# Optimization experiments

Measured on AMD Instinct MI355X. Metric: run time of the kernel, lower is better.

Reference implementation:

```python
import jax, jax.numpy as jnp
import numpy as np

DIM = 4096
NH = 32       # query heads
NKV = 8       # kv heads
HD = DIM // NH  # 128
B = 1
S = 2048
ROPE_BASE = 10000.0


def rope_tables(seq_len, head_dim, base=ROPE_BASE):
    inv_freq = 1.0 / base ** (jnp.arange(0, head_dim, 2, dtype=jnp.float32) / head_dim)
    t = jnp.arange(seq_len, dtype=jnp.float32)
    freqs = jnp.einsum('i,j->ij', t, inv_freq)          # [S, HD/2]
    emb = jnp.concatenate([freqs, freqs], axis=-1)      # [S, HD]
    return jnp.cos(emb), jnp.sin(emb)


def apply_rope(x, cos, sin):
    # x: [B, H, S, HD]; matches torch apply_rotary_emb (chunk halves)
    x1, x2 = jnp.split(x, 2, axis=-1)
    d = x1.shape[-1]
    c = cos[None, None, :, :d]
    s = sin[None, None, :, :d]
    return jnp.concatenate([x1 * c - x2 * s, x2 * c + x1 * s], axis=-1)


def setup_inputs() -> dict:
    key = jax.random.key(0)
    k0, k1, k2, k3, k4 = jax.random.split(key, 5)
    sc = 0.02  # typical init scale for stable softmax
    return {
        'x': jax.random.normal(k0, (B, S, DIM), jnp.float32),
        'wq': jax.random.normal(k1, (DIM, NH * HD), jnp.float32) * sc,
        'wk': jax.random.normal(k2, (DIM, NKV * HD), jnp.float32) * sc,
        'wv': jax.random.normal(k3, (DIM, NKV * HD), jnp.float32) * sc,
        'wo': jax.random.normal(k4, (NH * HD, DIM), jnp.float32) * sc,
        'mask': jnp.ones((1,), jnp.bool_),  # presence triggers is_causal=True in torch SDPA path
    }


def reference(x, wq, wk, wv, wo, mask):
    Bsz, Sl, _ = x.shape
    n_rep = NH // NKV
    q = (x @ wq).reshape(Bsz, Sl, NH, HD).transpose(0, 2, 1, 3)    # [B,NH,S,HD]
    k = (x @ wk).reshape(Bsz, Sl, NKV, HD).transpose(0, 2, 1, 3)   # [B,NKV,S,HD]
    v = (x @ wv).reshape(Bsz, Sl, NKV, HD).transpose(0, 2, 1, 3)
    cos, sin = rope_tables(Sl, HD)
    q = apply_rope(q, cos, sin)
    k = apply_rope(k, cos, sin)
    # GQA without repeat_interleave: group query heads per kv head
    qg = q.reshape(Bsz, NKV, n_rep, Sl, HD)
    scale = HD ** -0.5
    scores = jnp.einsum('bgrqd,bgkd->bgrqk', qg, k) * scale        # [B,NKV,n_rep,S,S]
    causal = jnp.tril(jnp.ones((Sl, Sl), dtype=bool))
    scores = jnp.where(causal[None, None, None], scores, jnp.finfo(scores.dtype).min)
    attn = jax.nn.softmax(scores, axis=-1)
    out = jnp.einsum('bgrqk,bgkd->bgrqd', attn, v)                 # [B,NKV,n_rep,S,HD]
    out = out.reshape(Bsz, NH, Sl, HD).transpose(0, 2, 1, 3).reshape(Bsz, Sl, NH * HD)
    return out @ wo
```

## Files before the change

kernel.cpp:

```cpp
#include <hip/hip_runtime.h>
#include <hip/hip_bf16.h>
#include <cstdint>
#include <cmath>

#define DIM 4096
#define NH 32
#define NKV 8
#define HD 128
#define S_LEN 2048
#define KVD (NKV * HD)
#define QS 6144
#define SCALE 0.08838834764831845f

typedef __attribute__((ext_vector_type(4))) float f32x4;
typedef __attribute__((ext_vector_type(8))) short short8;

__device__ __forceinline__ short f2bf(float f) {
  union { float f; uint32_t u; } v; v.f = f;
  uint32_t u = v.u;
  u += 0x7fffu + ((u >> 16) & 1u);
  return (short)(u >> 16);
}
__device__ __forceinline__ float bf2f(short b) {
  union { uint32_t u; float f; } v; v.u = ((uint32_t)(uint16_t)b) << 16;
  return v.f;
}

__device__ __forceinline__ void async16(const void* g, void* l) {
  __builtin_amdgcn_global_load_lds(
      (__attribute__((address_space(1))) void*)(g),
      (__attribute__((address_space(3))) void*)(l), 16, 0, 0);
}


__global__ void rope_tables_k(float* __restrict__ ct, float* __restrict__ st) {
  const int i = blockIdx.x * blockDim.x + threadIdx.x;
  if (i >= S_LEN * 64) return;
  const int s = i >> 6, d = i & 63;
  const float inv = powf(10000.0f, -(float)(2 * d) / 128.0f);
  const float fr = (float)s * inv;
  ct[i] = cosf(fr);
  st[i] = sinf(fr);
}

__global__ void cast_f32_bf16_k(const float* __restrict__ in, short* __restrict__ out, int n4) {
  const int i = blockIdx.x * blockDim.x + threadIdx.x;
  if (i >= n4) return;
  const float4 v = ((const float4*)in)[i];
  short4 o;
  o.x = f2bf(v.x); o.y = f2bf(v.y); o.z = f2bf(v.z); o.w = f2bf(v.w);
  ((short4*)out)[i] = o;
}

__global__ void transpose_cast_k(const float* __restrict__ wsrc, short* __restrict__ wt,
                                 int K, int N) {
  __shared__ float tile[32][33];
  const int tx = threadIdx.x, ty = threadIdx.y;
  const int c0 = blockIdx.x * 32, r0 = blockIdx.y * 32;
#pragma unroll
  for (int j = 0; j < 4; ++j)
    tile[ty + j * 8][tx] = wsrc[(size_t)(r0 + ty + j * 8) * N + c0 + tx];
  __syncthreads();
#pragma unroll
  for (int j = 0; j < 4; ++j)
    wt[(size_t)(c0 + ty + j * 8) * K + r0 + tx] = f2bf(tile[tx][ty + j * 8]);
}

__global__ void transpose_bf16_k(const short* __restrict__ in, short* __restrict__ out,
                                 int R, int C, int ldi) {
  __shared__ short tile[32][33];
  const int tx = threadIdx.x, ty = threadIdx.y;
  const int c0 = blockIdx.x * 32, r0 = blockIdx.y * 32;
#pragma unroll
  for (int j = 0; j < 4; ++j)
    tile[ty + j * 8][tx] = in[(size_t)(r0 + ty + j * 8) * ldi + c0 + tx];
  __syncthreads();
#pragma unroll
  for (int j = 0; j < 4; ++j)
    out[(size_t)(c0 + ty + j * 8) * R + r0 + tx] = tile[tx][ty + j * 8];
}

__global__ void rope_apply_k(short* __restrict__ xq, int ld, const float* __restrict__ ct,
                             const float* __restrict__ st, int nheads) {
  const int i = blockIdx.x * blockDim.x + threadIdx.x;
  const int total = S_LEN * nheads * 64;
  if (i >= total) return;
  const int d = i & 63;
  const int t = i >> 6;
  const int hh = t % nheads;
  const int s = t / nheads;
  short* p = xq + (size_t)s * ld + hh * HD + d;
  const float x1 = bf2f(p[0]);
  const float x2 = bf2f(p[64]);
  const float c = ct[(s << 6) + d];
  const float sn = st[(s << 6) + d];
  p[0]  = f2bf(x1 * c - x2 * sn);
  p[64] = f2bf(x2 * c + x1 * sn);
}


template <int BM, int NBUF, int OUT_BF16>
__global__ __launch_bounds__(512, 2) void gemm_p(
    const short* __restrict__ A, const short* __restrict__ BT,
    void* __restrict__ Cv, int M, int N, int K) {
  constexpr int TILE = (BM + 256) * 64;
  constexpr int LA = BM / 64;
  constexpr int L = LA + 4;
  constexpr int NP = BM / 64;
  __shared__ __attribute__((aligned(16))) short lds[NBUF][TILE];

  const int tid = threadIdx.x;
  const int w = tid >> 6, l = tid & 63;
  const int wr = w >> 2, wc = w & 3;
  const int lrow = l & 15, lg = l >> 4;

  int bid = blockIdx.x;
  const int cpx = gridDim.x >> 3;
  bid = (bid & 7) * cpx + (bid >> 3);
  const int ntn = N >> 8;
  const int m0 = (bid / ntn) * BM;
  const int n0 = (bid % ntn) << 8;

  auto stage = [&](int kt, int buf) {
    const int k0 = kt << 6;
    short* dst = &lds[buf][0];
#pragma unroll
    for (int it = 0; it < LA; ++it) {
      const int e = it * 512 + tid;
      const int row = e >> 3, j = e & 7;
      const int jsrc = j ^ (row & 7);
      async16(A + (size_t)(m0 + row) * K + k0 + jsrc * 8, dst + e * 8);
    }
#pragma unroll
    for (int it = 0; it < 4; ++it) {
      const int e = it * 512 + tid;
      const int row = e >> 3, j = e & 7;
      const int jsrc = j ^ (row & 7);
      async16(BT + (size_t)(n0 + row) * K + k0 + jsrc * 8, dst + BM * 64 + e * 8);
    }
  };

  auto vwait = [&](int J) {
    if constexpr (BM == 256) {
      if (J >= 1) asm volatile("s_waitcnt vmcnt(8)" ::: "memory");
      else        asm volatile("s_waitcnt vmcnt(0)" ::: "memory");
    } else {
      if (J >= 2)      asm volatile("s_waitcnt vmcnt(12)" ::: "memory");
      else if (J == 1) asm volatile("s_waitcnt vmcnt(6)" ::: "memory");
      else             asm volatile("s_waitcnt vmcnt(0)" ::: "memory");
    }
  };

  f32x4 acc[NP * 2][4] = {};

  const int KT = K >> 6;
#pragma unroll
  for (int t = 0; t < NBUF; ++t) stage(t, t);
  vwait(NBUF - 1);
  __builtin_amdgcn_s_barrier();

  for (int kt = 0; kt < KT; ++kt) {
    const int buf = kt % NBUF;
    const short* Ah = &lds[buf][0];
    const short* Bh = &lds[buf][BM * 64];
    short8 bfrag[2][4];

#pragma unroll
    for (int p = 0; p < NP; ++p) {
      short8 afrag[2][2];
#pragma unroll
      for (int mi = 0; mi < 2; ++mi) {
        const int row = wr * (BM / 2) + (p * 2 + mi) * 16 + lrow;
#pragma unroll
        for (int kk = 0; kk < 2; ++kk)
          afrag[mi][kk] =
              *(const short8*)(Ah + row * 64 + (((kk * 4 + lg) ^ (row & 7)) << 3));
      }
      if (p == 0) {
#pragma unroll
        for (int n = 0; n < 4; ++n) {
          const int row = wc * 64 + n * 16 + lrow;
#pragma unroll
          for (int kk = 0; kk < 2; ++kk)
            bfrag[kk][n] =
                *(const short8*)(Bh + row * 64 + (((kk * 4 + lg) ^ (row & 7)) << 3));
        }
      }
      __builtin_amdgcn_s_barrier();
      asm volatile("s_waitcnt lgkmcnt(0)" ::: "memory");
      __builtin_amdgcn_s_setprio(1);
#pragma unroll
      for (int kk = 0; kk < 2; ++kk)
#pragma unroll
        for (int mi = 0; mi < 2; ++mi)
#pragma unroll
          for (int n = 0; n < 4; ++n)
            acc[p * 2 + mi][n] = __builtin_amdgcn_mfma_f32_16x16x32_bf16(
                afrag[mi][kk], bfrag[kk][n], acc[p * 2 + mi][n], 0, 0, 0);
      __builtin_amdgcn_s_setprio(0);
      __builtin_amdgcn_s_barrier();
    }
    if (kt + 1 < KT) {
      const int nst = kt + NBUF;
      if (nst < KT) stage(nst, buf);
      const int J = (nst < KT ? nst : KT - 1) - (kt + 1);
      vwait(J);
      __builtin_amdgcn_s_barrier();
    }
  }

  const int orow0 = m0 + wr * (BM / 2) + lg * 4;
  const int ocol0 = n0 + wc * 64 + lrow;
#pragma unroll
  for (int m = 0; m < NP * 2; ++m)
#pragma unroll
    for (int n = 0; n < 4; ++n)
#pragma unroll
      for (int r = 0; r < 4; ++r) {
        const size_t idx = (size_t)(orow0 + m * 16 + r) * N + (ocol0 + n * 16);
        if (OUT_BF16)
          ((short*)Cv)[idx] = f2bf(acc[m][n][r]);
        else
          ((float*)Cv)[idx] = acc[m][n][r];
      }
}


__global__ __launch_bounds__(256, 2) void attn_k(
    const short* __restrict__ Q, const short* __restrict__ Kc,
    const short* __restrict__ VTg, short* __restrict__ O) {
  __shared__ __attribute__((aligned(16))) short Ks[2][64 * 128];
  __shared__ __attribute__((aligned(16))) short Vt[2][128 * 64];
  __shared__ __attribute__((aligned(16))) short Ps[4][32 * 64];

  const int tid = threadIdx.x;
  const int w = tid >> 6, l = tid & 63;
  const int lrow = l & 15, lg = l >> 4;

  int b = blockIdx.x, h, qt;
  if (b < 256) { h = b >> 3; qt = 15 - (b & 7); }
  else { b -= 256; h = b >> 3; qt = b & 7; }
  const int kvh = h >> 2;
  const int qb0 = qt * 128;
  const int qrow0 = qb0 + w * 32;
  const int nkt = 2 * qt + 2;

  short8 qf[2][4];
#pragma unroll
  for (int nq = 0; nq < 2; ++nq) {
    const short* qp = Q + (size_t)(qrow0 + nq * 16 + lrow) * QS + h * HD;
#pragma unroll
    for (int c = 0; c < 4; ++c) qf[nq][c] = *(const short8*)(qp + c * 32 + lg * 8);
  }

  f32x4 o_acc[2][8] = {};
  float m[2] = {-INFINITY, -INFINITY};
  float lsum[2] = {0.f, 0.f};

  auto stage = [&](int kb, int buf) {
    short* kd = Ks[buf];
    short* vd = Vt[buf];
#pragma unroll
    for (int it = 0; it < 4; ++it) {
      const int e = it * 256 + tid;
      const int row = e >> 4, j = e & 15;
      const int jsrc = (j & 8) | ((j ^ row) & 7);
      async16(Kc + (size_t)(kb + row) * QS + kvh * HD + jsrc * 8, kd + e * 8);
    }
#pragma unroll
    for (int it = 0; it < 4; ++it) {
      const int e = it * 256 + tid;
      const int d = e >> 3, j = e & 7;
      const int jsrc = (j ^ d) & 7;
      async16(VTg + (size_t)(kvh * HD + d) * S_LEN + kb + jsrc * 8, vd + e * 8);
    }
  };

  stage(0, 0);
  int cur = 0;

  for (int kt = 0; kt < nkt; ++kt) {
    __syncthreads();
    if (kt + 1 < nkt) stage((kt + 1) * 64, cur ^ 1);
    const int kb = kt * 64;

    if (kb <= qrow0 + 31) {
      const char* ks = (const char*)Ks[cur];
      const char* vt = (const char*)Vt[cur];
      char* psb = (char*)Ps[w];

      f32x4 stq[4][2] = {};
#pragma unroll
      for (int c = 0; c < 4; ++c) {
#pragma unroll
        for (int mk = 0; mk < 4; ++mk) {
          const short8 kf = *(const short8*)(
              ks + (mk * 16 + lrow) * 256 + (((c * 4 + lg) ^ (lrow & 7)) << 4));
          stq[mk][0] = __builtin_amdgcn_mfma_f32_16x16x32_bf16(kf, qf[0][c], stq[mk][0], 0, 0, 0);
          stq[mk][1] = __builtin_amdgcn_mfma_f32_16x16x32_bf16(kf, qf[1][c], stq[mk][1], 0, 0, 0);
        }
      }

      const bool needmask = (kb + 63 > qrow0);
#pragma unroll
      for (int mk = 0; mk < 4; ++mk)
#pragma unroll
        for (int nq = 0; nq < 2; ++nq)
#pragma unroll
          for (int r = 0; r < 4; ++r) {
            float v = stq[mk][nq][r] * SCALE;
            if (needmask && (kb + mk * 16 + lg * 4 + r > qrow0 + nq * 16 + lrow))
              v = -INFINITY;
            stq[mk][nq][r] = v;
          }

      float vmax[2];
#pragma unroll
      for (int nq = 0; nq < 2; ++nq) {
        float v = stq[0][nq][0];
#pragma unroll
        for (int mk = 0; mk < 4; ++mk)
#pragma unroll
          for (int r = 0; r < 4; ++r) v = fmaxf(v, stq[mk][nq][r]);
        v = fmaxf(v, __shfl_xor(v, 16));
        v = fmaxf(v, __shfl_xor(v, 32));
        vmax[nq] = v;
      }

      const int small = (vmax[0] <= m[0] + 8.0f) && (vmax[1] <= m[1] + 8.0f);
      if (!__all(small)) {
        float al[2];
#pragma unroll
        for (int nq = 0; nq < 2; ++nq) {
          const float mn = fmaxf(m[nq], vmax[nq]);
          al[nq] = __expf(m[nq] - mn);
          m[nq] = mn;
          lsum[nq] *= al[nq];
        }
#pragma unroll
        for (int mmq = 0; mmq < 2; ++mmq)
#pragma unroll
          for (int r = 0; r < 4; ++r) {
            const float a = __shfl(al[mmq], lg * 4 + r);
#pragma unroll
            for (int d = 0; d < 8; ++d) o_acc[mmq][d][r] *= a;
          }
      }

      float rs[2] = {0.f, 0.f};
#pragma unroll
      for (int nq = 0; nq < 2; ++nq) {
#pragma unroll
        for (int mk = 0; mk < 4; ++mk) {
          const float p0 = __expf(stq[mk][nq][0] - m[nq]);
          const float p1 = __expf(stq[mk][nq][1] - m[nq]);
          const float p2 = __expf(stq[mk][nq][2] - m[nq]);
          const float p3 = __expf(stq[mk][nq][3] - m[nq]);
          rs[nq] += (p0 + p1) + (p2 + p3);
          __hip_bfloat16 b0 = __float2bfloat16(p0), b1 = __float2bfloat16(p1);
          __hip_bfloat16 b2 = __float2bfloat16(p2), b3 = __float2bfloat16(p3);
          short4 pk;
          pk.x = *(short*)&b0; pk.y = *(short*)&b1; pk.z = *(short*)&b2; pk.w = *(short*)&b3;
          const int q = nq * 16 + lrow;
          *(short4*)(psb + q * 128 + ((mk * 32 + lg * 8) ^ ((q & 7) << 4))) = pk;
        }
        float r2 = rs[nq];
        r2 += __shfl_xor(r2, 16);
        r2 += __shfl_xor(r2, 32);
        lsum[nq] += r2;
      }

#pragma unroll
      for (int cc = 0; cc < 2; ++cc) {
        const int chunk = ((cc * 4 + lg) ^ (lrow & 7)) << 4;
        const short8 pa0 = *(const short8*)(psb + lrow * 128 + chunk);
        const short8 pa1 = *(const short8*)(psb + (16 + lrow) * 128 + chunk);
#pragma unroll
        for (int d = 0; d < 8; ++d) {
          const short8 vf = *(const short8*)(vt + (d * 16 + lrow) * 128 + chunk);
          o_acc[0][d] = __builtin_amdgcn_mfma_f32_16x16x32_bf16(pa0, vf, o_acc[0][d], 0, 0, 0);
          o_acc[1][d] = __builtin_amdgcn_mfma_f32_16x16x32_bf16(pa1, vf, o_acc[1][d], 0, 0, 0);
        }
      }
    }
    cur ^= 1;
  }

  float linv[2] = {1.0f / lsum[0], 1.0f / lsum[1]};
#pragma unroll
  for (int mmq = 0; mmq < 2; ++mmq)
#pragma unroll
    for (int r = 0; r < 4; ++r) {
      const float li = __shfl(linv[mmq], lg * 4 + r);
      short* op = O + (size_t)(qrow0 + mmq * 16 + lg * 4 + r) * DIM + h * HD;
#pragma unroll
      for (int d = 0; d < 8; ++d)
        op[d * 16 + lrow] = f2bf(o_acc[mmq][d][r] * li);
    }
}


extern "C" void kernel_launch(void* const* d_in, const int* in_sizes, int n_in,
                              void* d_out, int out_size, void* d_ws, size_t ws_size,
                              hipStream_t stream) {
  const float* x  = (const float*)d_in[0];
  const float* wq = (const float*)d_in[1];
  const float* wk = (const float*)d_in[2];
  const float* wv = (const float*)d_in[3];
  const float* wo = (const float*)d_in[4];
  float* out = (float*)d_out;
  (void)in_sizes; (void)n_in; (void)out_size; (void)ws_size;

  char* ws = (char*)d_ws;
  size_t off = 0;
  auto alloc = [&](size_t bytes) -> void* {
    void* p = ws + off;
    off += (bytes + 255) & ~(size_t)255;
    return p;
  };
  short* xb     = (short*)alloc((size_t)S_LEN * DIM * 2);
  short* wqkvT  = (short*)alloc((size_t)QS * DIM * 2);
  short* woT    = (short*)alloc((size_t)DIM * DIM * 2);
  short* qkv    = (short*)alloc((size_t)S_LEN * QS * 2);
  short* vtg    = (short*)alloc((size_t)KVD * S_LEN * 2);
  short* ao     = (short*)alloc((size_t)S_LEN * DIM * 2);
  float* ct     = (float*)alloc((size_t)S_LEN * 64 * 4);
  float* st     = (float*)alloc((size_t)S_LEN * 64 * 4);

  rope_tables_k<<<(S_LEN * 64) / 256, 256, 0, stream>>>(ct, st);
  cast_f32_bf16_k<<<(S_LEN * DIM / 4) / 256, 256, 0, stream>>>(x, xb, S_LEN * DIM / 4);
  transpose_cast_k<<<dim3(DIM / 32, DIM / 32), dim3(32, 8), 0, stream>>>(wq, wqkvT, DIM, DIM);
  transpose_cast_k<<<dim3(KVD / 32, DIM / 32), dim3(32, 8), 0, stream>>>(
      wk, wqkvT + (size_t)4096 * DIM, DIM, KVD);
  transpose_cast_k<<<dim3(KVD / 32, DIM / 32), dim3(32, 8), 0, stream>>>(
      wv, wqkvT + (size_t)5120 * DIM, DIM, KVD);
  transpose_cast_k<<<dim3(DIM / 32, DIM / 32), dim3(32, 8), 0, stream>>>(wo, woT, DIM, DIM);

  gemm_p<256, 2, 1><<<dim3((S_LEN / 256) * (QS / 256)), 512, 0, stream>>>(
      xb, wqkvT, qkv, S_LEN, QS, DIM);

  rope_apply_k<<<(S_LEN * NH * 64) / 256, 256, 0, stream>>>(qkv, QS, ct, st, NH);
  rope_apply_k<<<(S_LEN * NKV * 64) / 256, 256, 0, stream>>>(qkv + 4096, QS, ct, st, NKV);

  transpose_bf16_k<<<dim3(KVD / 32, S_LEN / 32), dim3(32, 8), 0, stream>>>(
      qkv + 5120, vtg, S_LEN, KVD, QS);

  attn_k<<<dim3(512), 256, 0, stream>>>(qkv, qkv + 4096, vtg, ao);

  gemm_p<128, 3, 0><<<dim3((S_LEN / 128) * (DIM / 256)), 512, 0, stream>>>(
      ao, woT, out, S_LEN, DIM, DIM);
}
```

Measured before the change: 372.8 us.

## Replace QKV projection GEMM with eight-phase ping-pong pipelined bf16 MFMA kernel

Adds a new 256x256-tile GEMM kernel for the fused QKV projection. It stages A and B half-tiles asynchronously into double-buffered LDS and splits each pair of K-steps into eight phases that interleave LDS fragment reads, global prefetch and MFMA quads. The phases are separated by barriers, and s_setprio raises priority during the MFMA sections. The goal is to hide global-load and LDS latency behind matrix-core work better than the generic gemm_p template. The cost is a hand-written waitcnt/barrier schedule that depends on K being a multiple of 128, and it is only used for the QKV GEMM.

```diff
diff --git a/kernel.cpp b/kernel.cpp
--- a/kernel.cpp
+++ b/kernel.cpp
@@ -99,13 +99,148 @@
 }
 
 
+#define PH(RD, ST, MF)                                         \
+  do {                                                         \
+    RD; ST;                                                    \
+    asm volatile("s_waitcnt vmcnt(6)" ::: "memory");           \
+    __builtin_amdgcn_s_barrier();                              \
+    asm volatile("s_waitcnt lgkmcnt(0)" ::: "memory");         \
+    __builtin_amdgcn_s_setprio(1);                             \
+    MF;                                                        \
+    __builtin_amdgcn_s_setprio(0);                             \
+    __builtin_amdgcn_s_barrier();                              \
+  } while (0)
+
+#define PHX(RD, ST, VW, MF)                                    \
+  do {                                                         \
+    RD; ST;                                                    \
+    VW;                                                        \
+    __builtin_amdgcn_s_barrier();                              \
+    asm volatile("s_waitcnt lgkmcnt(0)" ::: "memory");         \
+    __builtin_amdgcn_s_setprio(1);                             \
+    MF;                                                        \
+    __builtin_amdgcn_s_setprio(0);                             \
+    __builtin_amdgcn_s_barrier();                              \
+  } while (0)
+
+__global__ __launch_bounds__(512, 2) void gemm8p_k(
+    const short* __restrict__ A, const short* __restrict__ BT,
+    short* __restrict__ C, int M, int N, int K) {
+  __shared__ __attribute__((aligned(16))) short lds[2][2][2][128 * 64];
+  const int tid = threadIdx.x;
+  const int l = tid & 63, w = tid >> 6;
+  const int wr = w >> 2, wc = w & 3;
+  const int lrow = l & 15, lg = l >> 4;
+  const int brow0 = (wc & 1) * 64;
+
+  int bid = blockIdx.x;
+  const int cpx = gridDim.x >> 3;
+  bid = (bid & 7) * cpx + (bid >> 3);
+  const int ntn = N >> 8;
+  const int m0 = (bid / ntn) << 8;
+  const int n0 = (bid % ntn) << 8;
+
+  auto stageH = [&](int tau, int ab, int h) {
+    const short* src = ab ? BT : A;
+    const int base = (ab ? n0 : m0) + h * 128;
+    short* dst = &lds[tau & 1][ab][h][0];
+    const int k0 = tau << 6;
+    const int r0 = tid >> 3;
+    const int js = (tid & 7) ^ (r0 & 7);
+    async16(src + (size_t)(base + r0) * K + k0 + js * 8, dst + tid * 8);
+    async16(src + (size_t)(base + 64 + r0) * K + k0 + js * 8, dst + (512 + tid) * 8);
+  };
+  auto ldA = [&](short8 (&dst)[4][2], int b, int rh) {
+    const short* Ah = &lds[b][0][wr][0];
+#pragma unroll
+    for (int mi = 0; mi < 4; ++mi) {
+      const int row = rh * 64 + mi * 16 + lrow;
+#pragma unroll
+      for (int kk = 0; kk < 2; ++kk)
+        dst[mi][kk] = *(const short8*)(Ah + row * 64 + (((kk * 4 + lg) ^ (row & 7)) << 3));
+    }
+  };
+  auto ldB = [&](short8 (&dst)[2][2], int b, int ch) {
+    const short* Bh = &lds[b][1][wc >> 1][0];
+#pragma unroll
+    for (int ni = 0; ni < 2; ++ni) {
+      const int row = brow0 + ch * 32 + ni * 16 + lrow;
+#pragma unroll
+      for (int kk = 0; kk < 2; ++kk)
+        dst[ni][kk] = *(const short8*)(Bh + row * 64 + (((kk * 4 + lg) ^ (row & 7)) << 3));
+    }
+  };
+
+  f32x4 acc[8][4] = {};
+  auto quad = [&](int mr0, short8 (&Af)[4][2], int nc0, short8 (&Bf)[2][2]) {
+#pragma unroll
+    for (int kk = 0; kk < 2; ++kk)
+#pragma unroll
+      for (int mi = 0; mi < 4; ++mi)
+#pragma unroll
+        for (int ni = 0; ni < 2; ++ni)
+          acc[mr0 + mi][nc0 + ni] = __builtin_amdgcn_mfma_f32_16x16x32_bf16(
+              Af[mi][kk], Bf[ni][kk], acc[mr0 + mi][nc0 + ni], 0, 0, 0);
+  };
+
+  short8 Aa[4][2], Ab[4][2], Bc0A[2][2], Bc0B[2][2], Bc1[2][2];
+
+  stageH(0, 1, 0); stageH(0, 0, 0); stageH(0, 1, 1); stageH(0, 0, 1);
+  stageH(1, 1, 0); stageH(1, 0, 0);
+  asm volatile("s_waitcnt vmcnt(4)" ::: "memory");
+  __builtin_amdgcn_s_barrier();
+  ldB(Bc0A, 0, 0);
+  ldA(Aa, 0, 0);
+
+  const int KT = K >> 6;
+  for (int u = 0; u < (KT - 2) / 2; ++u) {
+    const int e = 2 * u, o = e + 1;
+    PH(ldB(Bc1, 0, 1),  stageH(o, 1, 1),     quad(0, Aa, 0, Bc0A));
+    PH(ldA(Ab, 0, 1),   stageH(o, 0, 1),     quad(0, Aa, 2, Bc1));
+    PH(ldB(Bc0B, 1, 0), stageH(e + 2, 1, 0), quad(4, Ab, 0, Bc0A));
+    PH(ldA(Aa, 1, 0),   stageH(e + 2, 0, 0), quad(4, Ab, 2, Bc1));
+    PH(ldB(Bc1, 1, 1),  stageH(o + 1, 1, 1), quad(0, Aa, 0, Bc0B));
+    PH(ldA(Ab, 1, 1),   stageH(o + 1, 0, 1), quad(0, Aa, 2, Bc1));
+    PH(ldB(Bc0A, 0, 0), stageH(o + 2, 1, 0), quad(4, Ab, 0, Bc0B));
+    PH(ldA(Aa, 0, 0),   stageH(o + 2, 0, 0), quad(4, Ab, 2, Bc1));
+  }
+
+  {
+    const int O = KT - 1;
+    PHX(ldB(Bc1, 0, 1),  stageH(O, 1, 1),
+        asm volatile("s_waitcnt vmcnt(6)" ::: "memory"), quad(0, Aa, 0, Bc0A));
+    PHX(ldA(Ab, 0, 1),   stageH(O, 0, 1),
+        asm volatile("s_waitcnt vmcnt(4)" ::: "memory"), quad(0, Aa, 2, Bc1));
+    PHX(ldB(Bc0B, 1, 0), (void)0,
+        asm volatile("s_waitcnt vmcnt(2)" ::: "memory"), quad(4, Ab, 0, Bc0A));
+    PHX(ldA(Aa, 1, 0),   (void)0,
+        asm volatile("s_waitcnt vmcnt(0)" ::: "memory"), quad(4, Ab, 2, Bc1));
+    ldB(Bc1, 1, 1);
+    quad(0, Aa, 0, Bc0B);
+    ldA(Ab, 1, 1);
+    quad(0, Aa, 2, Bc1);
+    quad(4, Ab, 0, Bc0B);
+    quad(4, Ab, 2, Bc1);
+  }
+
+  const int orow0 = m0 + wr * 128 + lg * 4;
+  const int ocol0 = n0 + wc * 64 + lrow;
+#pragma unroll
+  for (int m = 0; m < 8; ++m)
+#pragma unroll
+    for (int n = 0; n < 4; ++n)
+#pragma unroll
+      for (int r = 0; r < 4; ++r)
+        C[(size_t)(orow0 + m * 16 + r) * N + (ocol0 + n * 16)] = f2bf(acc[m][n][r]);
+}
+
+
 template <int BM, int NBUF, int OUT_BF16>
 __global__ __launch_bounds__(512, 2) void gemm_p(
     const short* __restrict__ A, const short* __restrict__ BT,
     void* __restrict__ Cv, int M, int N, int K) {
   constexpr int TILE = (BM + 256) * 64;
   constexpr int LA = BM / 64;
-  constexpr int L = LA + 4;
   constexpr int NP = BM / 64;
   __shared__ __attribute__((aligned(16))) short lds[NBUF][TILE];
 
@@ -436,7 +571,7 @@
       wv, wqkvT + (size_t)5120 * DIM, DIM, KVD);
   transpose_cast_k<<<dim3(DIM / 32, DIM / 32), dim3(32, 8), 0, stream>>>(wo, woT, DIM, DIM);
 
-  gemm_p<256, 2, 1><<<dim3((S_LEN / 256) * (QS / 256)), 512, 0, stream>>>(
+  gemm8p_k<<<dim3((S_LEN / 256) * (QS / 256)), 512, 0, stream>>>(
       xb, wqkvT, qkv, S_LEN, QS, DIM);
 
   rope_apply_k<<<(S_LEN * NH * 64) / 256, 256, 0, stream>>>(qkv, QS, ct, st, NH);
```

Result: slower. 578.5 us (+55.2%).

## Add ping-pong phased 256x256 GEMM kernel for QKV projection

Applied to the files above, without the earlier changes.

Adds a new bf16 GEMM kernel for the fused QKV projection. It splits each K-step into four phases that interleave LDS fragment reads and async global-to-LDS loads with MFMA quadrants. The phases are separated by barriers and s_setprio so that waves alternate between memory work and math work, and the LDS tiles use an XOR swizzle. The aim is to hide load latency behind MFMA better than the generic pipelined kernel, at the cost of more complex, hand-scheduled code that relies on exact waitcnt counts.

```diff
diff --git a/kernel.cpp b/kernel.cpp
--- a/kernel.cpp
+++ b/kernel.cpp
@@ -99,13 +99,184 @@
 }
 
 
+#define RD_A(DST, BASE, SUB)                                                     \
+  do {                                                                           \
+    _Pragma("unroll") for (int mi_ = 0; mi_ < 4; ++mi_) {                        \
+      _Pragma("unroll") for (int kk_ = 0; kk_ < 2; ++kk_)                        \
+        DST[mi_][kk_] = *(const short8*)((BASE) +                                \
+            ((SUB) * 64 + mi_ * 16 + lrow) * 64 + cofs[kk_]);                    \
+    }                                                                            \
+  } while (0)
+
+#define RD_B(DST, BASE, SUB)                                                     \
+  do {                                                                           \
+    _Pragma("unroll") for (int ni_ = 0; ni_ < 2; ++ni_) {                        \
+      _Pragma("unroll") for (int kk_ = 0; kk_ < 2; ++kk_)                        \
+        DST[ni_][kk_] = *(const short8*)((BASE) +                                \
+            (brow + (SUB) * 32 + ni_ * 16 + lrow) * 64 + cofs[kk_]);             \
+    }                                                                            \
+  } while (0)
+
+#define ST_AB(AB, TAU)                                                           \
+  do {                                                                           \
+    const int k0_ = (TAU) << 6;                                                  \
+    const short* src_ = (AB) ? BT : A;                                           \
+    const int b0_ = (AB) ? n0 : m0;                                              \
+    short* dst_ = &lds[(TAU) & 1][AB][0][0];                                     \
+    async16(src_ + (size_t)(b0_ + r0s) * K + k0_ + jss * 8, dst_ + tid * 8);     \
+    async16(src_ + (size_t)(b0_ + 64 + r0s) * K + k0_ + jss * 8,                 \
+            dst_ + (512 + tid) * 8);                                             \
+    async16(src_ + (size_t)(b0_ + 128 + r0s) * K + k0_ + jss * 8,                \
+            dst_ + (1024 + tid) * 8);                                            \
+    async16(src_ + (size_t)(b0_ + 192 + r0s) * K + k0_ + jss * 8,                \
+            dst_ + (1536 + tid) * 8);                                            \
+  } while (0)
+
+#define QUAD(M0, AF, N0, BF)                                                     \
+  do {                                                                           \
+    _Pragma("unroll") for (int kk_ = 0; kk_ < 2; ++kk_)                          \
+      _Pragma("unroll") for (int mi_ = 0; mi_ < 4; ++mi_)                        \
+        _Pragma("unroll") for (int ni_ = 0; ni_ < 2; ++ni_)                      \
+          acc[(M0) + mi_][(N0) + ni_] = __builtin_amdgcn_mfma_f32_16x16x32_bf16( \
+              AF[mi_][kk_], BF[ni_][kk_], acc[(M0) + mi_][(N0) + ni_], 0, 0, 0); \
+  } while (0)
+
+#define PH_SYNC_N(VM)                                            \
+  asm volatile("s_waitcnt vmcnt(" #VM ")" ::: "memory");         \
+  __builtin_amdgcn_s_barrier();                                  \
+  asm volatile("s_waitcnt lgkmcnt(0)" ::: "memory");             \
+  __builtin_amdgcn_sched_barrier(0);                             \
+  __builtin_amdgcn_s_setprio(1)
+
+#define PH_END()                                                 \
+  __builtin_amdgcn_s_setprio(0);                                 \
+  __builtin_amdgcn_sched_barrier(0);                             \
+  __builtin_amdgcn_s_barrier()
+
+__global__ __launch_bounds__(512, 2) void gemm8p_k(
+    const short* __restrict__ A, const short* __restrict__ BT,
+    short* __restrict__ C, int M, int N, int K) {
+  __shared__ __attribute__((aligned(16))) short lds[2][2][2][128 * 64];
+  const int tid = threadIdx.x;
+  const int l = tid & 63, w = tid >> 6;
+  const int wr = w >> 2, wc = w & 3;
+  const int lrow = l & 15, lg = l >> 4;
+  const int brow = (wc & 1) * 64;
+  const int cofs[2] = {(lg ^ (lrow & 7)) << 3, ((4 + lg) ^ (lrow & 7)) << 3};
+  const int r0s = tid >> 3;
+  const int jss = (tid & 7) ^ (r0s & 7);
+
+  int bid = blockIdx.x;
+  const int cpx = gridDim.x >> 3;
+  bid = (bid & 7) * cpx + (bid >> 3);
+  const int ntn = N >> 8;
+  const int m0 = (bid / ntn) << 8;
+  const int n0 = (bid % ntn) << 8;
+
+  f32x4 acc[8][4] = {};
+  short8 A0f[4][2], A1f[4][2], B0f[2][2], B1f[2][2];
+
+  ST_AB(1, 0); ST_AB(0, 0); ST_AB(1, 1); ST_AB(0, 1);
+  asm volatile("s_waitcnt vmcnt(8)" ::: "memory");
+  __builtin_amdgcn_s_barrier();
+  {
+    const short* LB0 = &lds[0][1][wc >> 1][0];
+    const short* LA0 = &lds[0][0][wr][0];
+    RD_B(B0f, LB0, 0);
+    RD_A(A0f, LA0, 0);
+  }
+
+  const int KT = K >> 6;
+  for (int tau = 0; tau < KT - 2; ++tau) {
+    const int c = tau & 1;
+    const short* LA = &lds[c][0][wr][0];
+    const short* LB = &lds[c][1][wc >> 1][0];
+    const short* LAn = &lds[c ^ 1][0][wr][0];
+    const short* LBn = &lds[c ^ 1][1][wc >> 1][0];
+
+    RD_A(A1f, LA, 1);
+    PH_SYNC_N(4);
+    QUAD(0, A0f, 0, B0f);
+    PH_END();
+
+    RD_B(B1f, LB, 1);
+    PH_SYNC_N(4);
+    QUAD(4, A1f, 0, B0f);
+    PH_END();
+
+    RD_B(B0f, LBn, 0);
+    ST_AB(1, tau + 2);
+    PH_SYNC_N(4);
+    QUAD(0, A0f, 2, B1f);
+    PH_END();
+
+    RD_A(A0f, LAn, 0);
+    ST_AB(0, tau + 2);
+    PH_SYNC_N(4);
+    QUAD(4, A1f, 2, B1f);
+    PH_END();
+  }
+
+  {
+    const int c = (KT - 2) & 1;
+    const short* LA = &lds[c][0][wr][0];
+    const short* LB = &lds[c][1][wc >> 1][0];
+    const short* LAn = &lds[c ^ 1][0][wr][0];
+    const short* LBn = &lds[c ^ 1][1][wc >> 1][0];
+
+    RD_A(A1f, LA, 1);
+    PH_SYNC_N(4);
+    QUAD(0, A0f, 0, B0f);
+    PH_END();
+
+    RD_B(B1f, LB, 1);
+    PH_SYNC_N(4);
+    QUAD(4, A1f, 0, B0f);
+    PH_END();
+
+    RD_B(B0f, LBn, 0);
+    PH_SYNC_N(0);
+    QUAD(0, A0f, 2, B1f);
+    PH_END();
+
+    RD_A(A0f, LAn, 0);
+    PH_SYNC_N(0);
+    QUAD(4, A1f, 2, B1f);
+    PH_END();
+  }
+
+  {
+    const int c = (KT - 1) & 1;
+    const short* LA = &lds[c][0][wr][0];
+    const short* LB = &lds[c][1][wc >> 1][0];
+    RD_A(A1f, LA, 1);
+    RD_B(B1f, LB, 1);
+    asm volatile("s_waitcnt lgkmcnt(0)" ::: "memory");
+    __builtin_amdgcn_sched_barrier(0);
+    QUAD(0, A0f, 0, B0f);
+    QUAD(4, A1f, 0, B0f);
+    QUAD(0, A0f, 2, B1f);
+    QUAD(4, A1f, 2, B1f);
+  }
+
+  const int orow0 = m0 + wr * 128 + lg * 4;
+  const int ocol0 = n0 + wc * 64 + lrow;
+#pragma unroll
+  for (int m = 0; m < 8; ++m)
+#pragma unroll
+    for (int n = 0; n < 4; ++n)
+#pragma unroll
+      for (int r = 0; r < 4; ++r)
+        C[(size_t)(orow0 + m * 16 + r) * N + (ocol0 + n * 16)] = f2bf(acc[m][n][r]);
+}
+
+
 template <int BM, int NBUF, int OUT_BF16>
 __global__ __launch_bounds__(512, 2) void gemm_p(
     const short* __restrict__ A, const short* __restrict__ BT,
     void* __restrict__ Cv, int M, int N, int K) {
   constexpr int TILE = (BM + 256) * 64;
   constexpr int LA = BM / 64;
-  constexpr int L = LA + 4;
   constexpr int NP = BM / 64;
   __shared__ __attribute__((aligned(16))) short lds[NBUF][TILE];
 
@@ -436,7 +607,7 @@
       wv, wqkvT + (size_t)5120 * DIM, DIM, KVD);
   transpose_cast_k<<<dim3(DIM / 32, DIM / 32), dim3(32, 8), 0, stream>>>(wo, woT, DIM, DIM);
 
-  gemm_p<256, 2, 1><<<dim3((S_LEN / 256) * (QS / 256)), 512, 0, stream>>>(
+  gemm8p_k<<<dim3((S_LEN / 256) * (QS / 256)), 512, 0, stream>>>(
       xb, wqkvT, qkv, S_LEN, QS, DIM);
 
   rope_apply_k<<<(S_LEN * NH * 64) / 256, 256, 0, stream>>>(qkv, QS, ct, st, NH);
```

After: 363.8 us. 1.02x faster.

## Use 256x192-tile pipelined GEMM for QKV projection and merge RoPE launches

Applied to the files above, without the earlier changes.

Replaces the QKV projection GEMM with a new kernel that uses 256x192 output tiles, giving 256 blocks over the 2048x6144 problem instead of 192. It also adds a double-buffered, phase-interleaved schedule with explicit waitcnt, barriers and setprio around the MFMA groups. The two RoPE launches are merged into one over 40 contiguous heads, since the K heads directly follow the Q heads. The attention kernel's launch bounds are raised to 3 blocks per CU, which may constrain registers and cause spills.

```diff
diff --git a/kernel.cpp b/kernel.cpp
--- a/kernel.cpp
+++ b/kernel.cpp
@@ -99,13 +99,141 @@
 }
 
 
+#define PH3_SYNC(VM)                                             \
+  asm volatile("s_waitcnt vmcnt(" #VM ")" ::: "memory");         \
+  __builtin_amdgcn_s_barrier();                                  \
+  asm volatile("s_waitcnt lgkmcnt(0)" ::: "memory");             \
+  __builtin_amdgcn_sched_barrier(0);                             \
+  __builtin_amdgcn_s_setprio(1)
+
+#define PH3_END()                                                \
+  __builtin_amdgcn_s_setprio(0);                                 \
+  __builtin_amdgcn_sched_barrier(0);                             \
+  __builtin_amdgcn_s_barrier()
+
+__global__ __launch_bounds__(512, 2) void gemm192_k(
+    const short* __restrict__ A, const short* __restrict__ BT,
+    short* __restrict__ C, int M, int N, int K) {
+  __shared__ __attribute__((aligned(16))) short ldsA[2][256 * 64];
+  __shared__ __attribute__((aligned(16))) short ldsB[2][192 * 64];
+  const int tid = threadIdx.x;
+  const int l = tid & 63, w = tid >> 6;
+  const int wrM = w >> 1, wcN = w & 1;
+  const int lrow = l & 15, lg = l >> 4;
+  const int cofs[2] = {(lg ^ (lrow & 7)) << 3, ((4 + lg) ^ (lrow & 7)) << 3};
+  (void)M;
+
+  int bid = blockIdx.x;
+  const int cpx = gridDim.x >> 3;
+  bid = (bid & 7) * cpx + (bid >> 3);
+  const int ntn = N / 192;
+  const int m0 = (bid / ntn) << 8;
+  const int n0 = (bid % ntn) * 192;
+
+  auto stage = [&](int tau) {
+    const int k0 = tau << 6;
+    short* bd = &ldsB[tau & 1][0];
+    short* ad = &ldsA[tau & 1][0];
+#pragma unroll
+    for (int it = 0; it < 3; ++it) {
+      const int e = it * 512 + tid;
+      const int row = e >> 3;
+      const int js = (e & 7) ^ (row & 7);
+      async16(BT + (size_t)(n0 + row) * K + k0 + js * 8, bd + e * 8);
+    }
+#pragma unroll
+    for (int it = 0; it < 4; ++it) {
+      const int e = it * 512 + tid;
+      const int row = e >> 3;
+      const int js = (e & 7) ^ (row & 7);
+      async16(A + (size_t)(m0 + row) * K + k0 + js * 8, ad + e * 8);
+    }
+  };
+  auto rdA = [&](short8 (&dst)[4][2], int b) {
+    const short* p = &ldsA[b][0];
+#pragma unroll
+    for (int mi = 0; mi < 4; ++mi) {
+      const int row = wrM * 64 + mi * 16 + lrow;
+#pragma unroll
+      for (int kk = 0; kk < 2; ++kk)
+        dst[mi][kk] = *(const short8*)(p + row * 64 + cofs[kk]);
+    }
+  };
+  auto rdB = [&](short8 (&dst)[2][2], int b, int pr) {
+    const short* p = &ldsB[b][0];
+#pragma unroll
+    for (int ni = 0; ni < 2; ++ni) {
+      const int row = wcN * 96 + pr * 32 + ni * 16 + lrow;
+#pragma unroll
+      for (int kk = 0; kk < 2; ++kk)
+        dst[ni][kk] = *(const short8*)(p + row * 64 + cofs[kk]);
+    }
+  };
+
+  f32x4 acc[4][6] = {};
+  auto third = [&](short8 (&Af)[4][2], int pr, short8 (&Bf)[2][2]) {
+#pragma unroll
+    for (int kk = 0; kk < 2; ++kk)
+#pragma unroll
+      for (int mi = 0; mi < 4; ++mi)
+#pragma unroll
+        for (int ni = 0; ni < 2; ++ni)
+          acc[mi][pr * 2 + ni] = __builtin_amdgcn_mfma_f32_16x16x32_bf16(
+              Af[mi][kk], Bf[ni][kk], acc[mi][pr * 2 + ni], 0, 0, 0);
+  };
+
+  short8 Aa[4][2], Ab[4][2], B0f[2][2], B1f[2][2], B2f[2][2];
+
+  stage(0); stage(1);
+  asm volatile("s_waitcnt vmcnt(7)" ::: "memory");
+  __builtin_amdgcn_s_barrier();
+  rdB(B0f, 0, 0);
+  rdA(Aa, 0);
+
+  const int KT = K >> 6;
+  for (int u = 0; u < (KT - 2) / 2; ++u) {
+    const int e = 2 * u;
+    rdB(B1f, 0, 1); rdB(B2f, 0, 2);
+    PH3_SYNC(7);  third(Aa, 0, B0f); PH3_END();
+    stage(e + 2);
+    PH3_SYNC(7);  third(Aa, 1, B1f); PH3_END();
+    rdB(B0f, 1, 0); rdA(Ab, 1);
+    PH3_SYNC(7);  third(Aa, 2, B2f); PH3_END();
+    rdB(B1f, 1, 1); rdB(B2f, 1, 2);
+    PH3_SYNC(7);  third(Ab, 0, B0f); PH3_END();
+    stage(e + 3);
+    PH3_SYNC(7);  third(Ab, 1, B1f); PH3_END();
+    rdB(B0f, 0, 0); rdA(Aa, 0);
+    PH3_SYNC(7);  third(Ab, 2, B2f); PH3_END();
+  }
+  rdB(B1f, 0, 1); rdB(B2f, 0, 2);
+  PH3_SYNC(7);  third(Aa, 0, B0f); PH3_END();
+  PH3_SYNC(0);  third(Aa, 1, B1f); PH3_END();
+  rdB(B0f, 1, 0); rdA(Ab, 1);
+  PH3_SYNC(0);  third(Aa, 2, B2f); PH3_END();
+  rdB(B1f, 1, 1); rdB(B2f, 1, 2);
+  PH3_SYNC(0);  third(Ab, 0, B0f); PH3_END();
+  PH3_SYNC(0);  third(Ab, 1, B1f); PH3_END();
+  PH3_SYNC(0);  third(Ab, 2, B2f); PH3_END();
+
+  const int orow0 = m0 + wrM * 64 + lg * 4;
+  const int ocol0 = n0 + wcN * 96 + lrow;
+#pragma unroll
+  for (int mi = 0; mi < 4; ++mi)
+#pragma unroll
+    for (int n = 0; n < 6; ++n)
+#pragma unroll
+      for (int r = 0; r < 4; ++r)
+        C[(size_t)(orow0 + mi * 16 + r) * N + (ocol0 + n * 16)] = f2bf(acc[mi][n][r]);
+}
+
+
 template <int BM, int NBUF, int OUT_BF16>
 __global__ __launch_bounds__(512, 2) void gemm_p(
     const short* __restrict__ A, const short* __restrict__ BT,
     void* __restrict__ Cv, int M, int N, int K) {
   constexpr int TILE = (BM + 256) * 64;
   constexpr int LA = BM / 64;
-  constexpr int L = LA + 4;
   constexpr int NP = BM / 64;
   __shared__ __attribute__((aligned(16))) short lds[NBUF][TILE];
 
@@ -226,7 +354,7 @@
 }
 
 
-__global__ __launch_bounds__(256, 2) void attn_k(
+__global__ __launch_bounds__(256, 3) void attn_k(
     const short* __restrict__ Q, const short* __restrict__ Kc,
     const short* __restrict__ VTg, short* __restrict__ O) {
   __shared__ __attribute__((aligned(16))) short Ks[2][64 * 128];
@@ -436,11 +564,10 @@
       wv, wqkvT + (size_t)5120 * DIM, DIM, KVD);
   transpose_cast_k<<<dim3(DIM / 32, DIM / 32), dim3(32, 8), 0, stream>>>(wo, woT, DIM, DIM);
 
-  gemm_p<256, 2, 1><<<dim3((S_LEN / 256) * (QS / 256)), 512, 0, stream>>>(
+  gemm192_k<<<dim3((S_LEN / 256) * (QS / 192)), 512, 0, stream>>>(
       xb, wqkvT, qkv, S_LEN, QS, DIM);
 
-  rope_apply_k<<<(S_LEN * NH * 64) / 256, 256, 0, stream>>>(qkv, QS, ct, st, NH);
-  rope_apply_k<<<(S_LEN * NKV * 64) / 256, 256, 0, stream>>>(qkv + 4096, QS, ct, st, NKV);
+  rope_apply_k<<<(S_LEN * 40 * 64) / 256, 256, 0, stream>>>(qkv, QS, ct, st, 40);
 
   transpose_bf16_k<<<dim3(KVD / 32, S_LEN / 32), dim3(32, 8), 0, stream>>>(
       qkv + 5120, vtg, S_LEN, KVD, QS);
```

Result: faster. 354.1 us (-5.0%).
